# Optimization experiments

Hardware: AMD Instinct MI355X
Metric: run time of the kernel (lower is better)

The kernel has to match this reference:

```python
import jax, jax.numpy as jnp
import numpy as np

N = 50000
E = 800000
F_IN = 128
HID = 64
G = 512
NEG_SLOPE = 0.2


def setup_inputs() -> dict:
    key = jax.random.key(0)
    ks = jax.random.split(key, 24)
    g = lambda i, shape: jax.random.normal(ks[i], shape, dtype=jnp.float32) * 0.1
    inp = {
        "x": jax.random.normal(ks[0], (N, F_IN), dtype=jnp.float32),
        "edge_index": jax.random.randint(ks[1], (2, E), 0, N),
        "edge_weight": jax.random.uniform(ks[2], (E, 1), dtype=jnp.float32),
        "batch": jnp.sort(jax.random.randint(ks[3], (N,), 0, G)),
        # layer 1
        "W1": g(4, (F_IN, HID)), "as1": g(5, (HID,)), "ad1": g(6, (HID,)),
        "We1": g(7, (1, HID)), "ae1": g(8, (HID,)), "b1": jnp.zeros((HID,), jnp.float32),
        # layer 2
        "W2": g(9, (HID, HID)), "as2": g(10, (HID,)), "ad2": g(11, (HID,)),
        "We2": g(12, (1, HID)), "ae2": g(13, (HID,)), "b2": jnp.zeros((HID,), jnp.float32),
        # layer 3
        "W3": g(14, (HID, HID)), "as3": g(15, (HID,)), "ad3": g(16, (HID,)),
        "We3": g(17, (1, HID)), "ae3": g(18, (HID,)), "b3": jnp.zeros((HID,), jnp.float32),
        # readout
        "lin_w": g(19, (HID, 1)), "lin_b": jnp.zeros((1,), jnp.float32),
    }
    return inp


def gat_layer(x, src, dst, eattr, W, att_s, att_d, We, att_e, bias):
    # x: [N,Fin]; src/dst: [Et]; eattr: [Et,1]
    h = x @ W                                  # [N,HID]
    a_src = h @ att_s                          # [N]
    a_dst = h @ att_d                          # [N]
    a_edge = (eattr @ We) @ att_e              # [Et]
    alpha = a_src[src] + a_dst[dst] + a_edge   # [Et]
    alpha = jax.nn.leaky_relu(alpha, NEG_SLOPE)
    # segment softmax over incoming edges of each dst node
    m = jax.ops.segment_max(alpha, dst, num_segments=N)
    alpha = jnp.exp(alpha - m[dst])
    s = jax.ops.segment_sum(alpha, dst, num_segments=N)
    alpha = alpha / (s[dst] + 1e-16)
    # weighted scatter-add of source features
    out = jax.ops.segment_sum(h[src] * alpha[:, None], dst, num_segments=N)
    return out + bias


def reference(x, edge_index, edge_weight, batch,
              W1, as1, ad1, We1, ae1, b1,
              W2, as2, ad2, We2, ae2, b2,
              W3, as3, ad3, We3, ae3, b3,
              lin_w, lin_b):
    # PyG GATConv default: add self-loops with edge_attr fill_value='mean'
    loop = jnp.arange(N)
    src = jnp.concatenate([edge_index[0], loop])
    dst = jnp.concatenate([edge_index[1], loop])
    mean_attr = jnp.mean(edge_weight, axis=0, keepdims=True)  # [1,1]
    eattr = jnp.concatenate([edge_weight, jnp.broadcast_to(mean_attr, (N, 1))], axis=0)

    h = gat_layer(x, src, dst, eattr, W1, as1, ad1, We1, ae1, b1)
    h = jax.nn.relu(h)
    h = gat_layer(h, src, dst, eattr, W2, as2, ad2, We2, ae2, b2)
    h = jax.nn.relu(h)
    h = gat_layer(h, src, dst, eattr, W3, as3, ad3, We3, ae3, b3)

    # global mean pool over graphs
    sums = jax.ops.segment_sum(h, batch, num_segments=G)          # [G,HID]
    counts = jax.ops.segment_sum(jnp.ones((N,), h.dtype), batch, num_segments=G)
    pooled = sums / jnp.maximum(counts, 1.0)[:, None]
    # dropout p=0.6 is identity at inference
    out = pooled @ lin_w + lin_b                                   # [G,1]
    return jax.nn.sigmoid(out)
```

## Files before the change

### kernel.cpp

```cpp
#include <hip/hip_runtime.h>
#include <math.h>

#define N_NODES 50000
#define N_EDGES 800000
#define F_IN_DIM 128
#define HID 64
#define NG 512
#define NEG 0.2f
#define SLICE ((N_NODES + 7) / 8)
#define EPB 2048
#define CAP 64
#define XGRID (((N_EDGES + EPB - 1) / EPB) * 8)
#define GGRID ((N_NODES + 63) / 64)

static __device__ __forceinline__ float wave_sum(float v) {
    for (int o = 32; o; o >>= 1) v += __shfl_xor(v, o, 64);
    return v;
}

static __device__ __forceinline__ unsigned short f2bf(float f) {
    union { float f; unsigned u; } v; v.f = f;
    unsigned r = (v.u + 0x7FFF + ((v.u >> 16) & 1)) >> 16;
    return (unsigned short)r;
}
static __device__ __forceinline__ float bf2f(unsigned short b) {
    union { unsigned u; float f; } v; v.u = ((unsigned)b) << 16;
    return v.f;
}

__global__ __launch_bounds__(256) void scatter_gemm1_k(
        const int* __restrict__ ei, const float* __restrict__ ew,
        int* __restrict__ deg, unsigned* __restrict__ bucket,
        uint2* __restrict__ ovf, int* __restrict__ ovf_cnt,
        float* __restrict__ mean_acc,
        const float* __restrict__ We1, const float* __restrict__ ae1,
        const float* __restrict__ We2, const float* __restrict__ ae2,
        const float* __restrict__ We3, const float* __restrict__ ae3,
        float* __restrict__ ce,
        const float* __restrict__ X, const float* __restrict__ W,
        const float* __restrict__ as_, const float* __restrict__ ad_,
        unsigned short* __restrict__ H, float* __restrict__ Asrc,
        float* __restrict__ Adst) {
    extern __shared__ float smem[];
    const int tid = threadIdx.x;

    if (blockIdx.x < XGRID) {
        int grp = blockIdx.x >> 3, slice = blockIdx.x & 7;
        int lo = slice * SLICE, hi = lo + SLICE;
        int base = grp * EPB;
        int off0 = base + (tid << 2);
        int off1 = off0 + 1024;
        const int* dstp = ei + N_EDGES;
        int4 d0 = make_int4(-1, -1, -1, -1), d1 = make_int4(-1, -1, -1, -1);
        if (off0 < N_EDGES) d0 = *(const int4*)(dstp + off0);
        if (off1 < N_EDGES) d1 = *(const int4*)(dstp + off1);

        float s = 0.f;
        if (slice == 0) {
            float4 w0 = {0, 0, 0, 0}, w1 = {0, 0, 0, 0};
            if (off0 < N_EDGES) w0 = *(const float4*)(ew + off0);
            if (off1 < N_EDGES) w1 = *(const float4*)(ew + off1);
            s = w0.x + w0.y + w0.z + w0.w + w1.x + w1.y + w1.z + w1.w;
        }

        const int dv[8] = {d0.x, d0.y, d0.z, d0.w, d1.x, d1.y, d1.z, d1.w};
        const int eo[8] = {off0, off0 + 1, off0 + 2, off0 + 3,
                           off1, off1 + 1, off1 + 2, off1 + 3};
        #pragma unroll
        for (int i = 0; i < 8; ++i) {
            int dst = dv[i];
            if (dst >= lo && dst < hi) {
                int e = eo[i];
                int src = ei[e];
                float w = ew[e];
                int pos = atomicAdd(&deg[dst], 1);
                unsigned entry = (unsigned)(src & 0xFFFF) | ((unsigned)f2bf(w) << 16);
                if (pos < CAP) bucket[(dst << 6) + pos] = entry;
                else { int op = atomicAdd(ovf_cnt, 1); ovf[op] = make_uint2((unsigned)dst, entry); }
            }
        }

        int lane = tid & 63, wv = tid >> 6;
        if (slice == 0) {
            s = wave_sum(s);
            if (lane == 0) smem[wv] = s;
            __syncthreads();
            if (tid == 0) atomicAdd(mean_acc, smem[0] + smem[1] + smem[2] + smem[3]);
        }
        if (blockIdx.x == 0 && wv >= 1) {
            const float* We = (wv == 1) ? We1 : (wv == 2) ? We2 : We3;
            const float* ae = (wv == 1) ? ae1 : (wv == 2) ? ae2 : ae3;
            float v = We[lane] * ae[lane];
            v = wave_sum(v);
            if (lane == 0) ce[wv - 1] = v;
        }
        return;
    }

    float* Xs = smem;
    float* Wt = smem + 64 * 17;
    const int tx = tid & 15, ty = tid >> 4;
    const int bid = blockIdx.x - XGRID;
    const int rowBase = bid * 64;

    float4 acc0 = {0,0,0,0}, acc1 = {0,0,0,0}, acc2 = {0,0,0,0}, acc3 = {0,0,0,0};
    const int xrow = tid >> 2;
    const int xkq  = tid & 3;
    const float4* W4 = (const float4*)W;
    float4* Wt4 = (float4*)Wt;

    #pragma unroll 2
    for (int kt = 0; kt < (F_IN_DIM >> 4); ++kt) {
        __syncthreads();
        int k0 = kt << 4;
        int grow = rowBase + xrow;
        float4 xv = {0,0,0,0};
        if (grow < N_NODES)
            xv = *(const float4*)(X + (size_t)grow * F_IN_DIM + k0 + (xkq << 2));
        float* xd = Xs + xrow * 17 + (xkq << 2);
        xd[0] = xv.x; xd[1] = xv.y; xd[2] = xv.z; xd[3] = xv.w;
        Wt4[tid] = W4[(kt << 8) + tid];
        __syncthreads();

        #pragma unroll
        for (int kk = 0; kk < 16; ++kk) {
            float4 b = *(const float4*)&Wt[kk * HID + (tx << 2)];
            float a0 = Xs[(ty * 4 + 0) * 17 + kk];
            float a1 = Xs[(ty * 4 + 1) * 17 + kk];
            float a2 = Xs[(ty * 4 + 2) * 17 + kk];
            float a3 = Xs[(ty * 4 + 3) * 17 + kk];
            acc0.x += a0 * b.x; acc0.y += a0 * b.y; acc0.z += a0 * b.z; acc0.w += a0 * b.w;
            acc1.x += a1 * b.x; acc1.y += a1 * b.y; acc1.z += a1 * b.z; acc1.w += a1 * b.w;
            acc2.x += a2 * b.x; acc2.y += a2 * b.y; acc2.z += a2 * b.z; acc2.w += a2 * b.w;
            acc3.x += a3 * b.x; acc3.y += a3 * b.y; acc3.z += a3 * b.z; acc3.w += a3 * b.w;
        }
    }

    float4 as4 = *(const float4*)(as_ + (tx << 2));
    float4 ad4 = *(const float4*)(ad_ + (tx << 2));
    float4 accs[4] = {acc0, acc1, acc2, acc3};
    #pragma unroll
    for (int i = 0; i < 4; ++i) {
        int row = rowBase + ty * 4 + i;
        if (row >= N_NODES) break;
        float4 a = accs[i];
        ushort4 hv;
        hv.x = f2bf(a.x); hv.y = f2bf(a.y); hv.z = f2bf(a.z); hv.w = f2bf(a.w);
        *(ushort4*)(H + (size_t)row * HID + (tx << 2)) = hv;
        float vs = a.x * as4.x + a.y * as4.y + a.z * as4.z + a.w * as4.w;
        float vd = a.x * ad4.x + a.y * ad4.y + a.z * ad4.z + a.w * ad4.w;
        #pragma unroll
        for (int o = 8; o; o >>= 1) { vs += __shfl_xor(vs, o, 64); vd += __shfl_xor(vd, o, 64); }
        if (tx == 0) { Asrc[row] = vs; Adst[row] = vd; }
    }
}

__global__ __launch_bounds__(256) void gemm_att_k(
        const float* __restrict__ X, int F,
        const float* __restrict__ W,
        const float* __restrict__ as_, const float* __restrict__ ad_,
        unsigned short* __restrict__ H, float* __restrict__ Asrc,
        float* __restrict__ Adst) {
    extern __shared__ float smem[];
    float* Ws = smem;
    float* Xs = smem + F * HID;
    const int tid = threadIdx.x;
    const int tx = tid & 15, ty = tid >> 4;
    const int rowBase = blockIdx.x * 64;

    {
        const float4* W4 = (const float4*)W;
        float4* Ws4 = (float4*)Ws;
        int n4 = (F * HID) >> 2;
        for (int i = tid; i < n4; i += 256) Ws4[i] = W4[i];
    }

    float4 acc0 = {0,0,0,0}, acc1 = {0,0,0,0}, acc2 = {0,0,0,0}, acc3 = {0,0,0,0};

    const int xrow = tid >> 2;
    const int xkq  = tid & 3;
    const int nkt = F >> 4;

    for (int kt = 0; kt < nkt; ++kt) {
        __syncthreads();
        int k0 = kt << 4;
        int grow = rowBase + xrow;
        float4 xv = {0,0,0,0};
        if (grow < N_NODES)
            xv = *(const float4*)(X + (size_t)grow * F + k0 + (xkq << 2));
        float* xd = Xs + xrow * 17 + (xkq << 2);
        xd[0] = xv.x; xd[1] = xv.y; xd[2] = xv.z; xd[3] = xv.w;
        __syncthreads();

        #pragma unroll
        for (int kk = 0; kk < 16; ++kk) {
            float4 b = *(const float4*)&Ws[(k0 + kk) * HID + (tx << 2)];
            float a0 = Xs[(ty * 4 + 0) * 17 + kk];
            float a1 = Xs[(ty * 4 + 1) * 17 + kk];
            float a2 = Xs[(ty * 4 + 2) * 17 + kk];
            float a3 = Xs[(ty * 4 + 3) * 17 + kk];
            acc0.x += a0 * b.x; acc0.y += a0 * b.y; acc0.z += a0 * b.z; acc0.w += a0 * b.w;
            acc1.x += a1 * b.x; acc1.y += a1 * b.y; acc1.z += a1 * b.z; acc1.w += a1 * b.w;
            acc2.x += a2 * b.x; acc2.y += a2 * b.y; acc2.z += a2 * b.z; acc2.w += a2 * b.w;
            acc3.x += a3 * b.x; acc3.y += a3 * b.y; acc3.z += a3 * b.z; acc3.w += a3 * b.w;
        }
    }

    float4 as4 = *(const float4*)(as_ + (tx << 2));
    float4 ad4 = *(const float4*)(ad_ + (tx << 2));
    float4 accs[4] = {acc0, acc1, acc2, acc3};
    #pragma unroll
    for (int i = 0; i < 4; ++i) {
        int row = rowBase + ty * 4 + i;
        if (row >= N_NODES) break;
        float4 a = accs[i];
        ushort4 hv;
        hv.x = f2bf(a.x); hv.y = f2bf(a.y); hv.z = f2bf(a.z); hv.w = f2bf(a.w);
        *(ushort4*)(H + (size_t)row * HID + (tx << 2)) = hv;
        float vs = a.x * as4.x + a.y * as4.y + a.z * as4.z + a.w * as4.w;
        float vd = a.x * ad4.x + a.y * ad4.y + a.z * ad4.z + a.w * ad4.w;
        #pragma unroll
        for (int o = 8; o; o >>= 1) { vs += __shfl_xor(vs, o, 64); vd += __shfl_xor(vd, o, 64); }
        if (tx == 0) { Asrc[row] = vs; Adst[row] = vd; }
    }
}

__global__ __launch_bounds__(256) void aggregate_k(
        const unsigned short* __restrict__ H, const int* __restrict__ degArr,
        const unsigned* __restrict__ bucket,
        const uint2* __restrict__ ovf, const int* __restrict__ ovf_cnt_p,
        const float* __restrict__ Asrc, const float* __restrict__ Adst,
        const float* __restrict__ ceArr, int ci,
        const float* __restrict__ mean_acc,
        const float* __restrict__ bias, float* __restrict__ Out,
        int do_relu) {
    __shared__ float lp[16][64];
    __shared__ int   ls[16][64];
    int wv = threadIdx.x >> 6, lane = threadIdx.x & 63;
    int qid = lane >> 4, qlane = lane & 15;
    int slot = wv * 4 + qid;
    int n = blockIdx.x * 16 + slot;
    if (n >= N_NODES) return;
    int deg = degArr[n];
    int start = n << 6;
    float c = ceArr[ci];
    float ad = Adst[n];
    float mv = mean_acc[0] * (1.0f / (float)N_EDGES);
    float4 acc = {0, 0, 0, 0};
    float denom;

    float a_self = Asrc[n] + ad + c * mv;
    a_self = (a_self > 0.f) ? a_self : NEG * a_self;
    float p_self = __expf(a_self);

    if (deg <= CAP) {
        float lsum = 0.f;
        #pragma unroll
        for (int t = 0; t < 4; ++t) {
            int j = qlane + (t << 4);
            float p = 0.f; int s = 0;
            if (j < deg) {
                unsigned e = bucket[start + j];
                s = e & 0xFFFF;
                float a = Asrc[s] + ad + c * bf2f((unsigned short)(e >> 16));
                a = (a > 0.f) ? a : NEG * a;
                p = __expf(a);
                lsum += p;
            }
            lp[slot][j] = p;
            ls[slot][j] = s;
        }
        if (qlane == 0) lsum += p_self;
        #pragma unroll
        for (int o = 1; o < 16; o <<= 1) lsum += __shfl_xor(lsum, o, 64);
        denom = lsum;
        __builtin_amdgcn_wave_barrier();
        int dpad = (deg + 7) & ~7;
        for (int j = 0; j < dpad; j += 8) {
            float4 p0 = *(float4*)&lp[slot][j];
            float4 p1 = *(float4*)&lp[slot][j + 4];
            int4 s0 = *(int4*)&ls[slot][j];
            int4 s1 = *(int4*)&ls[slot][j + 4];
            ushort4 r0 = *(const ushort4*)(H + (size_t)s0.x * HID + (qlane << 2));
            ushort4 r1 = *(const ushort4*)(H + (size_t)s0.y * HID + (qlane << 2));
            ushort4 r2 = *(const ushort4*)(H + (size_t)s0.z * HID + (qlane << 2));
            ushort4 r3 = *(const ushort4*)(H + (size_t)s0.w * HID + (qlane << 2));
            ushort4 r4 = *(const ushort4*)(H + (size_t)s1.x * HID + (qlane << 2));
            ushort4 r5 = *(const ushort4*)(H + (size_t)s1.y * HID + (qlane << 2));
            ushort4 r6 = *(const ushort4*)(H + (size_t)s1.z * HID + (qlane << 2));
            ushort4 r7 = *(const ushort4*)(H + (size_t)s1.w * HID + (qlane << 2));
            acc.x += p0.x*bf2f(r0.x) + p0.y*bf2f(r1.x) + p0.z*bf2f(r2.x) + p0.w*bf2f(r3.x)
                   + p1.x*bf2f(r4.x) + p1.y*bf2f(r5.x) + p1.z*bf2f(r6.x) + p1.w*bf2f(r7.x);
            acc.y += p0.x*bf2f(r0.y) + p0.y*bf2f(r1.y) + p0.z*bf2f(r2.y) + p0.w*bf2f(r3.y)
                   + p1.x*bf2f(r4.y) + p1.y*bf2f(r5.y) + p1.z*bf2f(r6.y) + p1.w*bf2f(r7.y);
            acc.z += p0.x*bf2f(r0.z) + p0.y*bf2f(r1.z) + p0.z*bf2f(r2.z) + p0.w*bf2f(r3.z)
                   + p1.x*bf2f(r4.z) + p1.y*bf2f(r5.z) + p1.z*bf2f(r6.z) + p1.w*bf2f(r7.z);
            acc.w += p0.x*bf2f(r0.w) + p0.y*bf2f(r1.w) + p0.z*bf2f(r2.w) + p0.w*bf2f(r3.w)
                   + p1.x*bf2f(r4.w) + p1.y*bf2f(r5.w) + p1.z*bf2f(r6.w) + p1.w*bf2f(r7.w);
        }
    } else {
        int novf = *ovf_cnt_p;
        float lsum = 0.f;
        #pragma unroll
        for (int t = 0; t < 4; ++t) {
            int j = qlane + (t << 4);
            unsigned e = bucket[start + j];
            int s = e & 0xFFFF;
            float a = Asrc[s] + ad + c * bf2f((unsigned short)(e >> 16));
            a = (a > 0.f) ? a : NEG * a;
            float p = __expf(a);
            lsum += p;
            lp[slot][j] = p;
            ls[slot][j] = s;
        }
        __builtin_amdgcn_wave_barrier();
        for (int j = 0; j < 64; j += 8) {
            float4 p0 = *(float4*)&lp[slot][j];
            float4 p1 = *(float4*)&lp[slot][j + 4];
            int4 s0 = *(int4*)&ls[slot][j];
            int4 s1 = *(int4*)&ls[slot][j + 4];
            ushort4 r0 = *(const ushort4*)(H + (size_t)s0.x * HID + (qlane << 2));
            ushort4 r1 = *(const ushort4*)(H + (size_t)s0.y * HID + (qlane << 2));
            ushort4 r2 = *(const ushort4*)(H + (size_t)s0.z * HID + (qlane << 2));
            ushort4 r3 = *(const ushort4*)(H + (size_t)s0.w * HID + (qlane << 2));
            ushort4 r4 = *(const ushort4*)(H + (size_t)s1.x * HID + (qlane << 2));
            ushort4 r5 = *(const ushort4*)(H + (size_t)s1.y * HID + (qlane << 2));
            ushort4 r6 = *(const ushort4*)(H + (size_t)s1.z * HID + (qlane << 2));
            ushort4 r7 = *(const ushort4*)(H + (size_t)s1.w * HID + (qlane << 2));
            acc.x += p0.x*bf2f(r0.x) + p0.y*bf2f(r1.x) + p0.z*bf2f(r2.x) + p0.w*bf2f(r3.x)
                   + p1.x*bf2f(r4.x) + p1.y*bf2f(r5.x) + p1.z*bf2f(r6.x) + p1.w*bf2f(r7.x);
            acc.y += p0.x*bf2f(r0.y) + p0.y*bf2f(r1.y) + p0.z*bf2f(r2.y) + p0.w*bf2f(r3.y)
                   + p1.x*bf2f(r4.y) + p1.y*bf2f(r5.y) + p1.z*bf2f(r6.y) + p1.w*bf2f(r7.y);
            acc.z += p0.x*bf2f(r0.z) + p0.y*bf2f(r1.z) + p0.z*bf2f(r2.z) + p0.w*bf2f(r3.z)
                   + p1.x*bf2f(r4.z) + p1.y*bf2f(r5.z) + p1.z*bf2f(r6.z) + p1.w*bf2f(r7.z);
            acc.w += p0.x*bf2f(r0.w) + p0.y*bf2f(r1.w) + p0.z*bf2f(r2.w) + p0.w*bf2f(r3.w)
                   + p1.x*bf2f(r4.w) + p1.y*bf2f(r5.w) + p1.z*bf2f(r6.w) + p1.w*bf2f(r7.w);
        }
        for (int i = 0; i < novf; ++i) {
            uint2 o = ovf[i];
            if ((int)o.x == n) {
                unsigned e = o.y;
                int s = e & 0xFFFF;
                float a = Asrc[s] + ad + c * bf2f((unsigned short)(e >> 16));
                a = (a > 0.f) ? a : NEG * a;
                float p = __expf(a);
                if (qlane == 0) lsum += p;
                ushort4 r = *(const ushort4*)(H + (size_t)s * HID + (qlane << 2));
                acc.x += p * bf2f(r.x); acc.y += p * bf2f(r.y);
                acc.z += p * bf2f(r.z); acc.w += p * bf2f(r.w);
            }
        }
        if (qlane == 0) lsum += p_self;
        #pragma unroll
        for (int o = 1; o < 16; o <<= 1) lsum += __shfl_xor(lsum, o, 64);
        denom = lsum;
    }

    {
        ushort4 r = *(const ushort4*)(H + (size_t)n * HID + (qlane << 2));
        acc.x += p_self * bf2f(r.x); acc.y += p_self * bf2f(r.y);
        acc.z += p_self * bf2f(r.z); acc.w += p_self * bf2f(r.w);
    }

    float inv = 1.f / (denom + 1e-16f);
    float4 b4 = *(const float4*)(bias + (qlane << 2));
    acc.x = acc.x * inv + b4.x;
    acc.y = acc.y * inv + b4.y;
    acc.z = acc.z * inv + b4.z;
    acc.w = acc.w * inv + b4.w;
    if (do_relu) {
        acc.x = fmaxf(acc.x, 0.f); acc.y = fmaxf(acc.y, 0.f);
        acc.z = fmaxf(acc.z, 0.f); acc.w = fmaxf(acc.w, 0.f);
    }
    *(float4*)(Out + (size_t)n * HID + (qlane << 2)) = acc;
}

__global__ __launch_bounds__(256) void pool_readout_k(
        const float* __restrict__ act, const int* __restrict__ batch,
        const float* __restrict__ lin_w, const float* __restrict__ lin_b,
        float* __restrict__ out) {
    int wv = threadIdx.x >> 6, lane = threadIdx.x & 63;
    int g = blockIdx.x * 4 + wv;
    if (g >= NG) return;
    int lo = 0, hi = N_NODES;
    while (lo < hi) { int m = (lo + hi) >> 1; if (batch[m] < g) lo = m + 1; else hi = m; }
    int start = lo;
    hi = N_NODES;
    while (lo < hi) { int m = (lo + hi) >> 1; if (batch[m] < g + 1) lo = m + 1; else hi = m; }
    int end = lo;
    float acc = 0.f;
    int n = start;
    for (; n + 4 <= end; n += 4) {
        float v0 = act[(size_t)n * HID + lane];
        float v1 = act[(size_t)(n + 1) * HID + lane];
        float v2 = act[(size_t)(n + 2) * HID + lane];
        float v3 = act[(size_t)(n + 3) * HID + lane];
        acc += v0 + v1 + v2 + v3;
    }
    for (; n < end; ++n) acc += act[(size_t)n * HID + lane];
    float cntf = (float)(end - start);
    float v = acc / fmaxf(cntf, 1.f) * lin_w[lane];
    v = wave_sum(v);
    if (lane == 0) {
        float z = v + lin_b[0];
        out[g] = 1.f / (1.f + __expf(-z));
    }
}

extern "C" void kernel_launch(void* const* d_in, const int* in_sizes, int n_in,
                              void* d_out, int out_size, void* d_ws, size_t ws_size,
                              hipStream_t stream) {
    const float* x     = (const float*)d_in[0];
    const int*   ei    = (const int*)d_in[1];
    const float* ew    = (const float*)d_in[2];
    const int*   batch = (const int*)d_in[3];
    const float* W1  = (const float*)d_in[4];
    const float* as1 = (const float*)d_in[5];
    const float* ad1 = (const float*)d_in[6];
    const float* We1 = (const float*)d_in[7];
    const float* ae1 = (const float*)d_in[8];
    const float* b1  = (const float*)d_in[9];
    const float* W2  = (const float*)d_in[10];
    const float* as2 = (const float*)d_in[11];
    const float* ad2 = (const float*)d_in[12];
    const float* We2 = (const float*)d_in[13];
    const float* ae2 = (const float*)d_in[14];
    const float* b2  = (const float*)d_in[15];
    const float* W3  = (const float*)d_in[16];
    const float* as3 = (const float*)d_in[17];
    const float* ad3 = (const float*)d_in[18];
    const float* We3 = (const float*)d_in[19];
    const float* ae3 = (const float*)d_in[20];
    const float* b3  = (const float*)d_in[21];
    const float* lin_w = (const float*)d_in[22];
    const float* lin_b = (const float*)d_in[23];
    float* out = (float*)d_out;

    char* w = (char*)d_ws;
    size_t off = 0;
    auto alloc = [&](size_t bytes) -> void* {
        void* p = w + off;
        off = (off + bytes + 255) & ~(size_t)255;
        return p;
    };
    int*   deg      = (int*)alloc(N_NODES * sizeof(int));
    float* mean_acc = (float*)alloc(sizeof(float));
    int*   ovf_cnt  = (int*)alloc(sizeof(int));
    size_t zero_bytes = off;
    float* ce      = (float*)alloc(4 * sizeof(float));
    unsigned* bucket = (unsigned*)alloc((size_t)N_NODES * CAP * sizeof(unsigned));
    uint2* ovf     = (uint2*)alloc((size_t)N_EDGES * sizeof(uint2));
    float* a_src   = (float*)alloc(N_NODES * sizeof(float));
    float* a_dst   = (float*)alloc(N_NODES * sizeof(float));
    unsigned short* hbuf = (unsigned short*)alloc((size_t)N_NODES * HID * sizeof(unsigned short));
    float* actA    = (float*)alloc((size_t)N_NODES * HID * sizeof(float));
    float* actB    = (float*)alloc((size_t)N_NODES * HID * sizeof(float));

    hipMemsetAsync(d_ws, 0, zero_bytes, stream);

    int agrid = (N_NODES + 15) / 16;
    size_t lds_f = (size_t)(64 * 17 + 16 * 64) * sizeof(float);
    size_t lds2  = (size_t)(HID * HID + 64 * 17) * sizeof(float);

    scatter_gemm1_k<<<XGRID + GGRID, 256, lds_f, stream>>>(
        ei, ew, deg, bucket, ovf, ovf_cnt, mean_acc,
        We1, ae1, We2, ae2, We3, ae3, ce,
        x, W1, as1, ad1, hbuf, a_src, a_dst);

    aggregate_k<<<agrid, 256, 0, stream>>>(hbuf, deg, bucket, ovf, ovf_cnt,
                                           a_src, a_dst, ce, 0, mean_acc, b1, actA, 1);
    gemm_att_k<<<GGRID, 256, lds2, stream>>>(actA, HID, W2, as2, ad2, hbuf, a_src, a_dst);
    aggregate_k<<<agrid, 256, 0, stream>>>(hbuf, deg, bucket, ovf, ovf_cnt,
                                           a_src, a_dst, ce, 1, mean_acc, b2, actB, 1);
    gemm_att_k<<<GGRID, 256, lds2, stream>>>(actB, HID, W3, as3, ad3, hbuf, a_src, a_dst);
    aggregate_k<<<agrid, 256, 0, stream>>>(hbuf, deg, bucket, ovf, ovf_cnt,
                                           a_src, a_dst, ce, 2, mean_acc, b3, actA, 0);

    pool_readout_k<<<NG / 4, 256, 0, stream>>>(actA, batch, lin_w, lin_b, out);
}
```

Measured before the change: 282.8 us.

## Fuse aggregation with next layer's GEMM and attention projection

Each of the first two aggregation kernels now also applies bias+ReLU and multiplies the resulting row by the next layer's weight matrix from LDS, writing bf16 H and the attention scalars directly. This removes the separate gemm_att launches and the fp32 activation round trip through global memory. Double-buffered H and attention arrays are added to avoid read/write hazards, and each block now loads a 16KB weight tile into LDS, which may reduce occupancy.

Result: faster. 267.2 us (-5.5%).

```diff
diff --git a/kernel.cpp b/kernel.cpp
--- a/kernel.cpp
+++ b/kernel.cpp
@@ -155,74 +155,191 @@
     }
 }
 
-__global__ __launch_bounds__(256) void gemm_att_k(
-        const float* __restrict__ X, int F,
-        const float* __restrict__ W,
-        const float* __restrict__ as_, const float* __restrict__ ad_,
-        unsigned short* __restrict__ H, float* __restrict__ Asrc,
-        float* __restrict__ Adst) {
-    extern __shared__ float smem[];
-    float* Ws = smem;
-    float* Xs = smem + F * HID;
+#define AGG_PHASE(ACC, DENOM)                                                   \
+    {                                                                           \
+        float a_self = Asrc[n] + ad + c * mv;                                   \
+        a_self = (a_self > 0.f) ? a_self : NEG * a_self;                        \
+        p_self = __expf(a_self);                                                \
+        if (deg <= CAP) {                                                       \
+            float lsum = 0.f;                                                   \
+            _Pragma("unroll")                                                   \
+            for (int t = 0; t < 4; ++t) {                                       \
+                int j = qlane + (t << 4);                                       \
+                float p = 0.f; int s = 0;                                       \
+                if (j < deg) {                                                  \
+                    unsigned e = bucket[start + j];                             \
+                    s = e & 0xFFFF;                                             \
+                    float a = Asrc[s] + ad + c * bf2f((unsigned short)(e >> 16));\
+                    a = (a > 0.f) ? a : NEG * a;                                \
+                    p = __expf(a);                                              \
+                    lsum += p;                                                  \
+                }                                                               \
+                lp[slot][j] = p;                                                \
+                ls[slot][j] = s;                                                \
+            }                                                                   \
+            if (qlane == 0) lsum += p_self;                                     \
+            _Pragma("unroll")                                                   \
+            for (int o = 1; o < 16; o <<= 1) lsum += __shfl_xor(lsum, o, 64);   \
+            DENOM = lsum;                                                       \
+            __builtin_amdgcn_wave_barrier();                                    \
+            int dpad = (deg + 7) & ~7;                                          \
+            for (int j = 0; j < dpad; j += 8) {                                 \
+                float4 p0 = *(float4*)&lp[slot][j];                             \
+                float4 p1 = *(float4*)&lp[slot][j + 4];                         \
+                int4 s0 = *(int4*)&ls[slot][j];                                 \
+                int4 s1 = *(int4*)&ls[slot][j + 4];                             \
+                ushort4 r0 = *(const ushort4*)(H + (size_t)s0.x * HID + (qlane << 2)); \
+                ushort4 r1 = *(const ushort4*)(H + (size_t)s0.y * HID + (qlane << 2)); \
+                ushort4 r2 = *(const ushort4*)(H + (size_t)s0.z * HID + (qlane << 2)); \
+                ushort4 r3 = *(const ushort4*)(H + (size_t)s0.w * HID + (qlane << 2)); \
+                ushort4 r4 = *(const ushort4*)(H + (size_t)s1.x * HID + (qlane << 2)); \
+                ushort4 r5 = *(const ushort4*)(H + (size_t)s1.y * HID + (qlane << 2)); \
+                ushort4 r6 = *(const ushort4*)(H + (size_t)s1.z * HID + (qlane << 2)); \
+                ushort4 r7 = *(const ushort4*)(H + (size_t)s1.w * HID + (qlane << 2)); \
+                ACC.x += p0.x*bf2f(r0.x) + p0.y*bf2f(r1.x) + p0.z*bf2f(r2.x) + p0.w*bf2f(r3.x) \
+                       + p1.x*bf2f(r4.x) + p1.y*bf2f(r5.x) + p1.z*bf2f(r6.x) + p1.w*bf2f(r7.x); \
+                ACC.y += p0.x*bf2f(r0.y) + p0.y*bf2f(r1.y) + p0.z*bf2f(r2.y) + p0.w*bf2f(r3.y) \
+                       + p1.x*bf2f(r4.y) + p1.y*bf2f(r5.y) + p1.z*bf2f(r6.y) + p1.w*bf2f(r7.y); \
+                ACC.z += p0.x*bf2f(r0.z) + p0.y*bf2f(r1.z) + p0.z*bf2f(r2.z) + p0.w*bf2f(r3.z) \
+                       + p1.x*bf2f(r4.z) + p1.y*bf2f(r5.z) + p1.z*bf2f(r6.z) + p1.w*bf2f(r7.z); \
+                ACC.w += p0.x*bf2f(r0.w) + p0.y*bf2f(r1.w) + p0.z*bf2f(r2.w) + p0.w*bf2f(r3.w) \
+                       + p1.x*bf2f(r4.w) + p1.y*bf2f(r5.w) + p1.z*bf2f(r6.w) + p1.w*bf2f(r7.w); \
+            }                                                                   \
+        } else {                                                                \
+            int novf = *ovf_cnt_p;                                              \
+            float lsum = 0.f;                                                   \
+            _Pragma("unroll")                                                   \
+            for (int t = 0; t < 4; ++t) {                                       \
+                int j = qlane + (t << 4);                                       \
+                unsigned e = bucket[start + j];                                 \
+                int s = e & 0xFFFF;                                             \
+                float a = Asrc[s] + ad + c * bf2f((unsigned short)(e >> 16));   \
+                a = (a > 0.f) ? a : NEG * a;                                    \
+                float p = __expf(a);                                            \
+                lsum += p;                                                      \
+                lp[slot][j] = p;                                                \
+                ls[slot][j] = s;                                                \
+            }                                                                   \
+            __builtin_amdgcn_wave_barrier();                                    \
+            for (int j = 0; j < 64; j += 8) {                                   \
+                float4 p0 = *(float4*)&lp[slot][j];                             \
+                float4 p1 = *(float4*)&lp[slot][j + 4];                         \
+                int4 s0 = *(int4*)&ls[slot][j];                                 \
+                int4 s1 = *(int4*)&ls[slot][j + 4];                             \
+                ushort4 r0 = *(const ushort4*)(H + (size_t)s0.x * HID + (qlane << 2)); \
+                ushort4 r1 = *(const ushort4*)(H + (size_t)s0.y * HID + (qlane << 2)); \
+                ushort4 r2 = *(const ushort4*)(H + (size_t)s0.z * HID + (qlane << 2)); \
+                ushort4 r3 = *(const ushort4*)(H + (size_t)s0.w * HID + (qlane << 2)); \
+                ushort4 r4 = *(const ushort4*)(H + (size_t)s1.x * HID + (qlane << 2)); \
+                ushort4 r5 = *(const ushort4*)(H + (size_t)s1.y * HID + (qlane << 2)); \
+                ushort4 r6 = *(const ushort4*)(H + (size_t)s1.z * HID + (qlane << 2)); \
+                ushort4 r7 = *(const ushort4*)(H + (size_t)s1.w * HID + (qlane << 2)); \
+                ACC.x += p0.x*bf2f(r0.x) + p0.y*bf2f(r1.x) + p0.z*bf2f(r2.x) + p0.w*bf2f(r3.x) \
+                       + p1.x*bf2f(r4.x) + p1.y*bf2f(r5.x) + p1.z*bf2f(r6.x) + p1.w*bf2f(r7.x); \
+                ACC.y += p0.x*bf2f(r0.y) + p0.y*bf2f(r1.y) + p0.z*bf2f(r2.y) + p0.w*bf2f(r3.y) \
+                       + p1.x*bf2f(r4.y) + p1.y*bf2f(r5.y) + p1.z*bf2f(r6.y) + p1.w*bf2f(r7.y); \
+                ACC.z += p0.x*bf2f(r0.z) + p0.y*bf2f(r1.z) + p0.z*bf2f(r2.z) + p0.w*bf2f(r3.z) \
+                       + p1.x*bf2f(r4.z) + p1.y*bf2f(r5.z) + p1.z*bf2f(r6.z) + p1.w*bf2f(r7.z); \
+                ACC.w += p0.x*bf2f(r0.w) + p0.y*bf2f(r1.w) + p0.z*bf2f(r2.w) + p0.w*bf2f(r3.w) \
+                       + p1.x*bf2f(r4.w) + p1.y*bf2f(r5.w) + p1.z*bf2f(r6.w) + p1.w*bf2f(r7.w); \
+            }                                                                   \
+            for (int i = 0; i < novf; ++i) {                                    \
+                uint2 o = ovf[i];                                               \
+                if ((int)o.x == n) {                                            \
+                    unsigned e = o.y;                                           \
+                    int s = e & 0xFFFF;                                         \
+                    float a = Asrc[s] + ad + c * bf2f((unsigned short)(e >> 16));\
+                    a = (a > 0.f) ? a : NEG * a;                                \
+                    float p = __expf(a);                                        \
+                    if (qlane == 0) lsum += p;                                  \
+                    ushort4 r = *(const ushort4*)(H + (size_t)s * HID + (qlane << 2)); \
+                    ACC.x += p * bf2f(r.x); ACC.y += p * bf2f(r.y);             \
+                    ACC.z += p * bf2f(r.z); ACC.w += p * bf2f(r.w);             \
+                }                                                               \
+            }                                                                   \
+            if (qlane == 0) lsum += p_self;                                     \
+            _Pragma("unroll")                                                   \
+            for (int o = 1; o < 16; o <<= 1) lsum += __shfl_xor(lsum, o, 64);   \
+            DENOM = lsum;                                                       \
+        }                                                                       \
+        ushort4 rr = *(const ushort4*)(H + (size_t)n * HID + (qlane << 2));     \
+        ACC.x += p_self * bf2f(rr.x); ACC.y += p_self * bf2f(rr.y);             \
+        ACC.z += p_self * bf2f(rr.z); ACC.w += p_self * bf2f(rr.w);             \
+    }
+
+__global__ __launch_bounds__(256) void agg_gemm_k(
+        const unsigned short* __restrict__ H, const int* __restrict__ degArr,
+        const unsigned* __restrict__ bucket,
+        const uint2* __restrict__ ovf, const int* __restrict__ ovf_cnt_p,
+        const float* __restrict__ Asrc, const float* __restrict__ Adst,
+        const float* __restrict__ ceArr, int ci,
+        const float* __restrict__ mean_acc,
+        const float* __restrict__ bias,
+        const float* __restrict__ Wn, const float* __restrict__ asn,
+        const float* __restrict__ adn,
+        unsigned short* __restrict__ H2, float* __restrict__ Asrc2,
+        float* __restrict__ Adst2) {
+    __shared__ float lp[16][64];
+    __shared__ int   ls[16][64];
+    __shared__ float Wl[64 * 64];
+    __shared__ float rowBuf[16][68];
     const int tid = threadIdx.x;
-    const int tx = tid & 15, ty = tid >> 4;
-    const int rowBase = blockIdx.x * 64;
+    int wv = tid >> 6, lane = tid & 63;
+    int qid = lane >> 4, qlane = lane & 15;
+    int slot = wv * 4 + qid;
+    int n = blockIdx.x * 16 + slot;
 
     {
-        const float4* W4 = (const float4*)W;
-        float4* Ws4 = (float4*)Ws;
-        int n4 = (F * HID) >> 2;
-        for (int i = tid; i < n4; i += 256) Ws4[i] = W4[i];
-    }
-
-    float4 acc0 = {0,0,0,0}, acc1 = {0,0,0,0}, acc2 = {0,0,0,0}, acc3 = {0,0,0,0};
-
-    const int xrow = tid >> 2;
-    const int xkq  = tid & 3;
-    const int nkt = F >> 4;
-
-    for (int kt = 0; kt < nkt; ++kt) {
-        __syncthreads();
-        int k0 = kt << 4;
-        int grow = rowBase + xrow;
-        float4 xv = {0,0,0,0};
-        if (grow < N_NODES)
-            xv = *(const float4*)(X + (size_t)grow * F + k0 + (xkq << 2));
-        float* xd = Xs + xrow * 17 + (xkq << 2);
-        xd[0] = xv.x; xd[1] = xv.y; xd[2] = xv.z; xd[3] = xv.w;
-        __syncthreads();
-
-        #pragma unroll
-        for (int kk = 0; kk < 16; ++kk) {
-            float4 b = *(const float4*)&Ws[(k0 + kk) * HID + (tx << 2)];
-            float a0 = Xs[(ty * 4 + 0) * 17 + kk];
-            float a1 = Xs[(ty * 4 + 1) * 17 + kk];
-            float a2 = Xs[(ty * 4 + 2) * 17 + kk];
-            float a3 = Xs[(ty * 4 + 3) * 17 + kk];
-            acc0.x += a0 * b.x; acc0.y += a0 * b.y; acc0.z += a0 * b.z; acc0.w += a0 * b.w;
-            acc1.x += a1 * b.x; acc1.y += a1 * b.y; acc1.z += a1 * b.z; acc1.w += a1 * b.w;
-            acc2.x += a2 * b.x; acc2.y += a2 * b.y; acc2.z += a2 * b.z; acc2.w += a2 * b.w;
-            acc3.x += a3 * b.x; acc3.y += a3 * b.y; acc3.z += a3 * b.z; acc3.w += a3 * b.w;
-        }
-    }
-
-    float4 as4 = *(const float4*)(as_ + (tx << 2));
-    float4 ad4 = *(const float4*)(ad_ + (tx << 2));
-    float4 accs[4] = {acc0, acc1, acc2, acc3};
+        const float4* W4 = (const float4*)Wn;
+        float4* Wl4 = (float4*)Wl;
+        for (int i = tid; i < (HID * HID) >> 2; i += 256) Wl4[i] = W4[i];
+    }
+
+    int deg = degArr[n];
+    int start = n << 6;
+    float c = ceArr[ci];
+    float ad = Adst[n];
+    float mv = mean_acc[0] * (1.0f / (float)N_EDGES);
+    float4 acc = {0, 0, 0, 0};
+    float denom, p_self;
+
+    AGG_PHASE(acc, denom)
+
+    float inv = 1.f / (denom + 1e-16f);
+    float4 b4 = *(const float4*)(bias + (qlane << 2));
+    acc.x = fmaxf(acc.x * inv + b4.x, 0.f);
+    acc.y = fmaxf(acc.y * inv + b4.y, 0.f);
+    acc.z = fmaxf(acc.z * inv + b4.z, 0.f);
+    acc.w = fmaxf(acc.w * inv + b4.w, 0.f);
+    *(float4*)&rowBuf[slot][qlane << 2] = acc;
+    __syncthreads();
+
+    float4 h2 = {0, 0, 0, 0};
     #pragma unroll
-    for (int i = 0; i < 4; ++i) {
-        int row = rowBase + ty * 4 + i;
-        if (row >= N_NODES) break;
-        float4 a = accs[i];
-        ushort4 hv;
-        hv.x = f2bf(a.x); hv.y = f2bf(a.y); hv.z = f2bf(a.z); hv.w = f2bf(a.w);
-        *(ushort4*)(H + (size_t)row * HID + (tx << 2)) = hv;
-        float vs = a.x * as4.x + a.y * as4.y + a.z * as4.z + a.w * as4.w;
-        float vd = a.x * ad4.x + a.y * ad4.y + a.z * ad4.z + a.w * ad4.w;
-        #pragma unroll
-        for (int o = 8; o; o >>= 1) { vs += __shfl_xor(vs, o, 64); vd += __shfl_xor(vd, o, 64); }
-        if (tx == 0) { Asrc[row] = vs; Adst[row] = vd; }
-    }
+    for (int k4 = 0; k4 < 16; ++k4) {
+        float4 a4 = *(const float4*)&rowBuf[slot][k4 << 2];
+        const float* wb = &Wl[(k4 << 2) * HID + (qlane << 2)];
+        float4 w0 = *(const float4*)(wb);
+        float4 w1 = *(const float4*)(wb + HID);
+        float4 w2 = *(const float4*)(wb + 2 * HID);
+        float4 w3 = *(const float4*)(wb + 3 * HID);
+        h2.x += a4.x*w0.x + a4.y*w1.x + a4.z*w2.x + a4.w*w3.x;
+        h2.y += a4.x*w0.y + a4.y*w1.y + a4.z*w2.y + a4.w*w3.y;
+        h2.z += a4.x*w0.z + a4.y*w1.z + a4.z*w2.z + a4.w*w3.z;
+        h2.w += a4.x*w0.w + a4.y*w1.w + a4.z*w2.w + a4.w*w3.w;
+    }
+
+    ushort4 hv;
+    hv.x = f2bf(h2.x); hv.y = f2bf(h2.y); hv.z = f2bf(h2.z); hv.w = f2bf(h2.w);
+    *(ushort4*)(H2 + (size_t)n * HID + (qlane << 2)) = hv;
+
+    float4 as4 = *(const float4*)(asn + (qlane << 2));
+    float4 ad4 = *(const float4*)(adn + (qlane << 2));
+    float vs = h2.x * as4.x + h2.y * as4.y + h2.z * as4.z + h2.w * as4.w;
+    float vd = h2.x * ad4.x + h2.y * ad4.y + h2.z * ad4.z + h2.w * ad4.w;
+    #pragma unroll
+    for (int o = 8; o; o >>= 1) { vs += __shfl_xor(vs, o, 64); vd += __shfl_xor(vd, o, 64); }
+    if (qlane == 0) { Asrc2[n] = vs; Adst2[n] = vd; }
 }
 
 __global__ __launch_bounds__(256) void aggregate_k(
@@ -232,8 +349,7 @@
         const float* __restrict__ Asrc, const float* __restrict__ Adst,
         const float* __restrict__ ceArr, int ci,
         const float* __restrict__ mean_acc,
-        const float* __restrict__ bias, float* __restrict__ Out,
-        int do_relu) {
+        const float* __restrict__ bias, float* __restrict__ Out) {
     __shared__ float lp[16][64];
     __shared__ int   ls[16][64];
     int wv = threadIdx.x >> 6, lane = threadIdx.x & 63;
@@ -247,120 +363,9 @@
     float ad = Adst[n];
     float mv = mean_acc[0] * (1.0f / (float)N_EDGES);
     float4 acc = {0, 0, 0, 0};
-    float denom;
-
-    float a_self = Asrc[n] + ad + c * mv;
-    a_self = (a_self > 0.f) ? a_self : NEG * a_self;
-    float p_self = __expf(a_self);
-
-    if (deg <= CAP) {
-        float lsum = 0.f;
-        #pragma unroll
-        for (int t = 0; t < 4; ++t) {
-            int j = qlane + (t << 4);
-            float p = 0.f; int s = 0;
-            if (j < deg) {
-                unsigned e = bucket[start + j];
-                s = e & 0xFFFF;
-                float a = Asrc[s] + ad + c * bf2f((unsigned short)(e >> 16));
-                a = (a > 0.f) ? a : NEG * a;
-                p = __expf(a);
-                lsum += p;
-            }
-            lp[slot][j] = p;
-            ls[slot][j] = s;
-        }
-        if (qlane == 0) lsum += p_self;
-        #pragma unroll
-        for (int o = 1; o < 16; o <<= 1) lsum += __shfl_xor(lsum, o, 64);
-        denom = lsum;
-        __builtin_amdgcn_wave_barrier();
-        int dpad = (deg + 7) & ~7;
-        for (int j = 0; j < dpad; j += 8) {
-            float4 p0 = *(float4*)&lp[slot][j];
-            float4 p1 = *(float4*)&lp[slot][j + 4];
-            int4 s0 = *(int4*)&ls[slot][j];
-            int4 s1 = *(int4*)&ls[slot][j + 4];
-            ushort4 r0 = *(const ushort4*)(H + (size_t)s0.x * HID + (qlane << 2));
-            ushort4 r1 = *(const ushort4*)(H + (size_t)s0.y * HID + (qlane << 2));
-            ushort4 r2 = *(const ushort4*)(H + (size_t)s0.z * HID + (qlane << 2));
-            ushort4 r3 = *(const ushort4*)(H + (size_t)s0.w * HID + (qlane << 2));
-            ushort4 r4 = *(const ushort4*)(H + (size_t)s1.x * HID + (qlane << 2));
-            ushort4 r5 = *(const ushort4*)(H + (size_t)s1.y * HID + (qlane << 2));
-            ushort4 r6 = *(const ushort4*)(H + (size_t)s1.z * HID + (qlane << 2));
-            ushort4 r7 = *(const ushort4*)(H + (size_t)s1.w * HID + (qlane << 2));
-            acc.x += p0.x*bf2f(r0.x) + p0.y*bf2f(r1.x) + p0.z*bf2f(r2.x) + p0.w*bf2f(r3.x)
-                   + p1.x*bf2f(r4.x) + p1.y*bf2f(r5.x) + p1.z*bf2f(r6.x) + p1.w*bf2f(r7.x);
-            acc.y += p0.x*bf2f(r0.y) + p0.y*bf2f(r1.y) + p0.z*bf2f(r2.y) + p0.w*bf2f(r3.y)
-                   + p1.x*bf2f(r4.y) + p1.y*bf2f(r5.y) + p1.z*bf2f(r6.y) + p1.w*bf2f(r7.y);
-            acc.z += p0.x*bf2f(r0.z) + p0.y*bf2f(r1.z) + p0.z*bf2f(r2.z) + p0.w*bf2f(r3.z)
-                   + p1.x*bf2f(r4.z) + p1.y*bf2f(r5.z) + p1.z*bf2f(r6.z) + p1.w*bf2f(r7.z);
-            acc.w += p0.x*bf2f(r0.w) + p0.y*bf2f(r1.w) + p0.z*bf2f(r2.w) + p0.w*bf2f(r3.w)
-                   + p1.x*bf2f(r4.w) + p1.y*bf2f(r5.w) + p1.z*bf2f(r6.w) + p1.w*bf2f(r7.w);
-        }
-    } else {
-        int novf = *ovf_cnt_p;
-        float lsum = 0.f;
-        #pragma unroll
-        for (int t = 0; t < 4; ++t) {
-            int j = qlane + (t << 4);
-            unsigned e = bucket[start + j];
-            int s = e & 0xFFFF;
-            float a = Asrc[s] + ad + c * bf2f((unsigned short)(e >> 16));
-            a = (a > 0.f) ? a : NEG * a;
-            float p = __expf(a);
-            lsum += p;
-            lp[slot][j] = p;
-            ls[slot][j] = s;
-        }
-        __builtin_amdgcn_wave_barrier();
-        for (int j = 0; j < 64; j += 8) {
-            float4 p0 = *(float4*)&lp[slot][j];
-            float4 p1 = *(float4*)&lp[slot][j + 4];
-            int4 s0 = *(int4*)&ls[slot][j];
-            int4 s1 = *(int4*)&ls[slot][j + 4];
-            ushort4 r0 = *(const ushort4*)(H + (size_t)s0.x * HID + (qlane << 2));
-            ushort4 r1 = *(const ushort4*)(H + (size_t)s0.y * HID + (qlane << 2));
-            ushort4 r2 = *(const ushort4*)(H + (size_t)s0.z * HID + (qlane << 2));
-            ushort4 r3 = *(const ushort4*)(H + (size_t)s0.w * HID + (qlane << 2));
-            ushort4 r4 = *(const ushort4*)(H + (size_t)s1.x * HID + (qlane << 2));
-            ushort4 r5 = *(const ushort4*)(H + (size_t)s1.y * HID + (qlane << 2));
-            ushort4 r6 = *(const ushort4*)(H + (size_t)s1.z * HID + (qlane << 2));
-            ushort4 r7 = *(const ushort4*)(H + (size_t)s1.w * HID + (qlane << 2));
-            acc.x += p0.x*bf2f(r0.x) + p0.y*bf2f(r1.x) + p0.z*bf2f(r2.x) + p0.w*bf2f(r3.x)
-                   + p1.x*bf2f(r4.x) + p1.y*bf2f(r5.x) + p1.z*bf2f(r6.x) + p1.w*bf2f(r7.x);
-            acc.y += p0.x*bf2f(r0.y) + p0.y*bf2f(r1.y) + p0.z*bf2f(r2.y) + p0.w*bf2f(r3.y)
-                   + p1.x*bf2f(r4.y) + p1.y*bf2f(r5.y) + p1.z*bf2f(r6.y) + p1.w*bf2f(r7.y);
-            acc.z += p0.x*bf2f(r0.z) + p0.y*bf2f(r1.z) + p0.z*bf2f(r2.z) + p0.w*bf2f(r3.z)
-                   + p1.x*bf2f(r4.z) + p1.y*bf2f(r5.z) + p1.z*bf2f(r6.z) + p1.w*bf2f(r7.z);
-            acc.w += p0.x*bf2f(r0.w) + p0.y*bf2f(r1.w) + p0.z*bf2f(r2.w) + p0.w*bf2f(r3.w)
-                   + p1.x*bf2f(r4.w) + p1.y*bf2f(r5.w) + p1.z*bf2f(r6.w) + p1.w*bf2f(r7.w);
-        }
-        for (int i = 0; i < novf; ++i) {
-            uint2 o = ovf[i];
-            if ((int)o.x == n) {
-                unsigned e = o.y;
-                int s = e & 0xFFFF;
-                float a = Asrc[s] + ad + c * bf2f((unsigned short)(e >> 16));
-                a = (a > 0.f) ? a : NEG * a;
-                float p = __expf(a);
-                if (qlane == 0) lsum += p;
-                ushort4 r = *(const ushort4*)(H + (size_t)s * HID + (qlane << 2));
-                acc.x += p * bf2f(r.x); acc.y += p * bf2f(r.y);
-                acc.z += p * bf2f(r.z); acc.w += p * bf2f(r.w);
-            }
-        }
-        if (qlane == 0) lsum += p_self;
-        #pragma unroll
-        for (int o = 1; o < 16; o <<= 1) lsum += __shfl_xor(lsum, o, 64);
-        denom = lsum;
-    }
-
-    {
-        ushort4 r = *(const ushort4*)(H + (size_t)n * HID + (qlane << 2));
-        acc.x += p_self * bf2f(r.x); acc.y += p_self * bf2f(r.y);
-        acc.z += p_self * bf2f(r.z); acc.w += p_self * bf2f(r.w);
-    }
+    float denom, p_self;
+
+    AGG_PHASE(acc, denom)
 
     float inv = 1.f / (denom + 1e-16f);
     float4 b4 = *(const float4*)(bias + (qlane << 2));
@@ -368,10 +373,6 @@
     acc.y = acc.y * inv + b4.y;
     acc.z = acc.z * inv + b4.z;
     acc.w = acc.w * inv + b4.w;
-    if (do_relu) {
-        acc.x = fmaxf(acc.x, 0.f); acc.y = fmaxf(acc.y, 0.f);
-        acc.z = fmaxf(acc.z, 0.f); acc.w = fmaxf(acc.w, 0.f);
-    }
     *(float4*)(Out + (size_t)n * HID + (qlane << 2)) = acc;
 }
 
@@ -452,29 +453,32 @@
     uint2* ovf     = (uint2*)alloc((size_t)N_EDGES * sizeof(uint2));
     float* a_src   = (float*)alloc(N_NODES * sizeof(float));
     float* a_dst   = (float*)alloc(N_NODES * sizeof(float));
-    unsigned short* hbuf = (unsigned short*)alloc((size_t)N_NODES * HID * sizeof(unsigned short));
+    float* a_src2  = (float*)alloc(N_NODES * sizeof(float));
+    float* a_dst2  = (float*)alloc(N_NODES * sizeof(float));
+    unsigned short* hbuf  = (unsigned short*)alloc((size_t)N_NODES * HID * sizeof(unsigned short));
+    unsigned short* hbuf2 = (unsigned short*)alloc((size_t)N_NODES * HID * sizeof(unsigned short));
     float* actA    = (float*)alloc((size_t)N_NODES * HID * sizeof(float));
-    float* actB    = (float*)alloc((size_t)N_NODES * HID * sizeof(float));
 
     hipMemsetAsync(d_ws, 0, zero_bytes, stream);
 
     int agrid = (N_NODES + 15) / 16;
     size_t lds_f = (size_t)(64 * 17 + 16 * 64) * sizeof(float);
-    size_t lds2  = (size_t)(HID * HID + 64 * 17) * sizeof(float);
 
     scatter_gemm1_k<<<XGRID + GGRID, 256, lds_f, stream>>>(
         ei, ew, deg, bucket, ovf, ovf_cnt, mean_acc,
         We1, ae1, We2, ae2, We3, ae3, ce,
         x, W1, as1, ad1, hbuf, a_src, a_dst);
 
+    agg_gemm_k<<<agrid, 256, 0, stream>>>(hbuf, deg, bucket, ovf, ovf_cnt,
+                                          a_src, a_dst, ce, 0, mean_acc, b1,
+                                          W2, as2, ad2, hbuf2, a_src2, a_dst2);
+
+    agg_gemm_k<<<agrid, 256, 0, stream>>>(hbuf2, deg, bucket, ovf, ovf_cnt,
+                                          a_src2, a_dst2, ce, 1, mean_acc, b2,
+                                          W3, as3, ad3, hbuf, a_src, a_dst);
+
     aggregate_k<<<agrid, 256, 0, stream>>>(hbuf, deg, bucket, ovf, ovf_cnt,
-                                           a_src, a_dst, ce, 0, mean_acc, b1, actA, 1);
-    gemm_att_k<<<GGRID, 256, lds2, stream>>>(actA, HID, W2, as2, ad2, hbuf, a_src, a_dst);
-    aggregate_k<<<agrid, 256, 0, stream>>>(hbuf, deg, bucket, ovf, ovf_cnt,
-                                           a_src, a_dst, ce, 1, mean_acc, b2, actB, 1);
-    gemm_att_k<<<GGRID, 256, lds2, stream>>>(actB, HID, W3, as3, ad3, hbuf, a_src, a_dst);
-    aggregate_k<<<agrid, 256, 0, stream>>>(hbuf, deg, bucket, ovf, ovf_cnt,
-                                           a_src, a_dst, ce, 2, mean_acc, b3, actA, 0);
+                                           a_src, a_dst, ce, 2, mean_acc, b3, actA);
 
     pool_readout_k<<<NG / 4, 256, 0, stream>>>(actA, batch, lin_w, lin_b, out);
 }
```
